# Performance work log

Hardware: AMD Instinct MI355X
Metric: run time of the kernel (lower is better)

## Reference

```python
import jax, jax.numpy as jnp
import numpy as np

B, QL, VL, HID, NH, CH = 16, 512, 512, 1024, 4, 10
DIM = HID // NH  # 256


def setup_inputs() -> dict:
    key = jax.random.key(0)
    ks = jax.random.split(key, 16)
    n = lambda k, s, sc=0.02: jax.random.normal(k, s, jnp.float32) * sc
    return {
        "query": jax.random.normal(ks[0], (B, QL, HID), jnp.float32),
        "value": jax.random.normal(ks[1], (B, VL, HID), jnp.float32),
        "prev_attn": jax.nn.softmax(jax.random.normal(ks[2], (B * NH, VL), jnp.float32), axis=-1),
        "conv_w": n(ks[3], (CH, 1, 3)),          # conv1d weight (out, in, k)
        "conv_b": jnp.zeros((CH,), jnp.float32),
        "Wq": n(ks[4], (HID, HID)), "bq": jnp.zeros((HID,), jnp.float32),  # query_projection
        "Wv": n(ks[5], (HID, HID)),               # value_projection (no bias)
        "Wloc": n(ks[6], (CH, DIM)),              # loc_projection (no bias)
        "bias": jax.random.uniform(ks[7], (HID,), jnp.float32, -0.1, 0.1),
        "Wout": n(ks[8], (2 * HID, HID)), "bout": jnp.zeros((HID,), jnp.float32),
        "swq": n(ks[9], (DIM, DIM)), "sbq": jnp.zeros((DIM,), jnp.float32),
        "swk": n(ks[10], (DIM, DIM)), "sbk": jnp.zeros((DIM,), jnp.float32),
        "swv": n(ks[11], (DIM, DIM)), "sbv": jnp.zeros((DIM,), jnp.float32),
    }


def _forward(query, value, prev_attn, conv_w, conv_b, Wq, bq, Wv, Wloc, bias,
             Wout, bout, swq, sbq, swk, sbk, swv, sbv):
    # location energy: conv1d over prev alignment, then per-head linear
    conv = jax.lax.conv_general_dilated(
        prev_attn[:, None, :], conv_w, window_strides=(1,), padding=((1, 1),),
        dimension_numbers=("NCH", "OIH", "NCH")) + conv_b[None, :, None]  # (B*NH, CH, VL)
    conv = conv.reshape(B, NH, CH, VL).transpose(0, 1, 3, 2)              # (B, NH, VL, CH)
    loc = jnp.einsum("bhvc,cd->bhvd", conv, Wloc)                         # (B, NH, VL, DIM)
    loc = loc.transpose(0, 2, 1, 3).reshape(B, VL, HID)                   # (B, VL, HID)

    q = query @ Wq + bq                                                   # (B, QL, HID)
    v = value @ Wv + loc + bias                                           # (B, VL, HID)

    # split heads: (B, L, NH, DIM) -> (NH*B, L, DIM)
    qh = q.reshape(B, QL, NH, DIM).transpose(2, 0, 1, 3).reshape(NH * B, QL, DIM)
    vh = v.reshape(B, VL, NH, DIM).transpose(2, 0, 1, 3).reshape(NH * B, VL, DIM)

    # scaled dot-product attention with key = value = vh (intended call)
    qq = qh @ swq + sbq
    kk = vh @ swk + sbk
    vv = vh @ swv + sbv
    scores = jnp.einsum("nqd,nkd->nqk", qq, kk) / np.float32(np.sqrt(DIM))
    attn = jax.nn.softmax(scores, axis=-1)                                # (NH*B, QL, VL)
    ctx = jnp.einsum("nqk,nkd->nqd", attn, vv)

    # merge heads: (NH, B, QL, DIM) -> (B, QL, HID)
    ctx = ctx.reshape(NH, B, QL, DIM).transpose(1, 2, 0, 3).reshape(B, QL, HID)

    combined = jnp.concatenate([ctx, query], axis=2)                      # (B, QL, 2*HID)
    out = jnp.tanh(combined @ Wout + bout)                                # (B, QL, HID)
    return out, attn


def reference(query, value, prev_attn, conv_w, conv_b, Wq, bq, Wv, Wloc, bias,
              Wout, bout, swq, sbq, swk, sbk, swv, sbv):
    return _forward(query, value, prev_attn, conv_w, conv_b, Wq, bq, Wv, Wloc,
                    bias, Wout, bout, swq, sbq, swk, sbk, swv, sbv)
```

## Files before the change

kernel.cpp:

```cpp
#include <hip/hip_runtime.h>
#include <math.h>

#define B_   16
#define QL_  512
#define VL_  512
#define HID_ 1024
#define NH_  4
#define CH_  10
#define DIM_ 256

typedef __attribute__((ext_vector_type(4))) float f32x4;
typedef __attribute__((ext_vector_type(8))) short bf16x8;

__device__ __forceinline__ ushort f2bf(float f) {
    union { float f; uint32_t u; } c; c.f = f;
    uint32_t u = c.u;
    u += 0x7fffu + ((u >> 16) & 1u);
    return (ushort)(u >> 16);
}

__device__ __forceinline__ void gload16(const void* g, void* l) {
    __builtin_amdgcn_global_load_lds((const __attribute__((address_space(1))) void*)g,
                                     (__attribute__((address_space(3))) void*)l,
                                     16, 0, 0);
}

__global__ __launch_bounds__(256)
void gemm_bf16(const ushort* __restrict__ A, const ushort* __restrict__ Bt,
               void* __restrict__ Cv, void* __restrict__ Cv2,
               const float* __restrict__ bias,
               int K, int lda, int ldb, int ldc,
               long long a1, long long a2, long long b1, long long b2,
               long long c1, long long c2, int WB,
               float post_scale, int flags)
{
    __shared__ ushort As[2][128 * 64];
    __shared__ ushort Bs[2][128 * 64];

    int z = blockIdx.z;
    int zm = z % WB, zd = z / WB;
    A  += a1 * zm + a2 * zd;
    Bt += b1 * zm + b2 * zd;
    long long coff = c1 * (long long)zm + c2 * (long long)zd;

    int gx = gridDim.x;
    int nwg = gx * gridDim.y;
    int flat = blockIdx.y * gx + blockIdx.x;
    int q = nwg >> 3, r = nwg & 7;
    int xcd = flat & 7, idx = flat >> 3;
    int logical = (xcd < r ? xcd * (q + 1) : r * (q + 1) + (xcd - r) * q) + idx;
    int brow = (logical / gx) * 128;
    int bcol = (logical % gx) * 128;

    int t = threadIdx.x;
    int lane = t & 63, w = t >> 6;
    int wr = (w >> 1) * 64, wc = (w & 1) * 64;

    int srow  = t >> 3;
    int sslot = t & 7;
    int sk = ((sslot ^ (srow & 7)) << 3);
    const ushort* gaBase = A  + (long long)(brow + srow) * lda + sk;
    const ushort* gbBase = Bt + (long long)(bcol + srow) * ldb + sk;

    f32x4 acc[4][4] = {};

    auto stage = [&](int buf, int k0) {
        ushort* la = &As[buf][t * 8];
        ushort* lb = &Bs[buf][t * 8];
        #pragma unroll
        for (int i = 0; i < 4; ++i) {
            gload16(gaBase + (long long)(i * 32) * lda + k0, la + i * 2048);
            gload16(gbBase + (long long)(i * 32) * ldb + k0, lb + i * 2048);
        }
    };

    int NT = K >> 6;
    stage(0, 0);
    __syncthreads();
    int cur = 0;
    for (int tI = 0; tI < NT; ++tI) {
        if (tI + 1 < NT) stage(cur ^ 1, (tI + 1) << 6);
        #pragma unroll
        for (int kk = 0; kk < 2; ++kk) {
            int slot = ((kk << 2) + (lane >> 4)) ^ (lane & 7);
            const ushort* ab = &As[cur][(wr + (lane & 15)) * 64 + slot * 8];
            const ushort* bb = &Bs[cur][(wc + (lane & 15)) * 64 + slot * 8];
            bf16x8 af[4], bfr[4];
            #pragma unroll
            for (int m = 0; m < 4; ++m) af[m]  = *(const bf16x8*)(ab + m * 1024);
            #pragma unroll
            for (int n = 0; n < 4; ++n) bfr[n] = *(const bf16x8*)(bb + n * 1024);
            #pragma unroll
            for (int m = 0; m < 4; ++m)
                #pragma unroll
                for (int n = 0; n < 4; ++n)
                    acc[m][n] = __builtin_amdgcn_mfma_f32_16x16x32_bf16(af[m], bfr[n], acc[m][n], 0, 0, 0);
        }
        __syncthreads();
        cur ^= 1;
    }

    float*  Cf = (float*)Cv + coff;
    ushort* Cb = (ushort*)Cv + coff;
    ushort* C2 = (ushort*)Cv2;
    #pragma unroll
    for (int m = 0; m < 4; ++m) {
        int r0 = brow + wr + m * 16 + (lane >> 4) * 4;
        #pragma unroll
        for (int n = 0; n < 4; ++n) {
            int c = bcol + wc + n * 16 + (lane & 15);
            float bv = bias ? bias[c] : 0.0f;
            float v0 = (acc[m][n][0] + bv) * post_scale;
            float v1 = (acc[m][n][1] + bv) * post_scale;
            float v2 = (acc[m][n][2] + bv) * post_scale;
            float v3 = (acc[m][n][3] + bv) * post_scale;
            if (flags & 2) { v0 = tanhf(v0); v1 = tanhf(v1); v2 = tanhf(v2); v3 = tanhf(v3); }
            if ((flags & 8) && c >= 1024) {
                ushort4 o;
                o.x = f2bf(v0); o.y = f2bf(v1); o.z = f2bf(v2); o.w = f2bf(v3);
                *(ushort4*)&C2[(long long)(c - 1024) * 8192 + r0] = o;
            } else if (flags & 1) {
                Cb[(long long)(r0 + 0) * ldc + c] = f2bf(v0);
                Cb[(long long)(r0 + 1) * ldc + c] = f2bf(v1);
                Cb[(long long)(r0 + 2) * ldc + c] = f2bf(v2);
                Cb[(long long)(r0 + 3) * ldc + c] = f2bf(v3);
            } else {
                Cf[(long long)(r0 + 0) * ldc + c] = v0;
                Cf[(long long)(r0 + 1) * ldc + c] = v1;
                Cf[(long long)(r0 + 2) * ldc + c] = v2;
                Cf[(long long)(r0 + 3) * ldc + c] = v3;
            }
        }
    }
}

__global__ __launch_bounds__(256)
void vext_fill_conv(const float* __restrict__ prev, const float* __restrict__ cw,
                    const float* __restrict__ cb, ushort* __restrict__ vext)
{
    int idx = blockIdx.x * 256 + threadIdx.x;
    int row = idx >> 6, j = idx & 63;
    int b = row >> 9, l = row & 511;
    ushort v = 0;
    if (j < 40) {
        int h = j / 10, c = j - h * 10;
        const float* p = prev + (long long)(b * 4 + h) * VL_;
        float xm = (l > 0)       ? p[l - 1] : 0.f;
        float x0 = p[l];
        float xp = (l < VL_ - 1) ? p[l + 1] : 0.f;
        v = f2bf(xm * cw[c * 3 + 0] + x0 * cw[c * 3 + 1] + xp * cw[c * 3 + 2] + cb[c]);
    }
    vext[(long long)row * 1088 + 1024 + j] = v;
}

__global__ __launch_bounds__(256)
void fold_small(const float* __restrict__ bq, const float* __restrict__ sbq, const float* __restrict__ swq,
                const float* __restrict__ bias, const float* __restrict__ sbk, const float* __restrict__ swk,
                const float* __restrict__ sbv, const float* __restrict__ swv,
                const float* __restrict__ Wloc,
                float* __restrict__ bqq, float* __restrict__ bkv,
                float* __restrict__ wlK, float* __restrict__ wlV)
{
    int idx = blockIdx.x * 256 + threadIdx.x;
    if (idx < 1024) {
        int h = idx >> 8, d = idx & 255;
        float s = 0.f;
        for (int j = 0; j < 256; ++j) s += bq[h * 256 + j] * swq[j * 256 + d];
        bqq[idx] = s + sbq[d];
    } else if (idx < 3072) {
        int i = idx - 1024;
        int kv = i >> 10, ii = i & 1023;
        int h = ii >> 8, d = ii & 255;
        const float* sw = kv ? swv : swk;
        const float* sb = kv ? sbv : sbk;
        float s = 0.f;
        for (int j = 0; j < 256; ++j) s += bias[h * 256 + j] * sw[j * 256 + d];
        bkv[i] = s + sb[d];
    } else if (idx < 5632) {
        int i = idx - 3072; int c = i >> 8, d = i & 255;
        float s = 0.f;
        for (int j = 0; j < 256; ++j) s += Wloc[c * 256 + j] * swk[j * 256 + d];
        wlK[i] = s;
    } else if (idx < 8192) {
        int i = idx - 5632; int c = i >> 8, d = i & 255;
        float s = 0.f;
        for (int j = 0; j < 256; ++j) s += Wloc[c * 256 + j] * swv[j * 256 + d];
        wlV[i] = s;
    }
}

__global__ __launch_bounds__(256)
void cast_rows(const float* __restrict__ in, ushort* __restrict__ out, int ld_out)
{
    long long idx = (long long)blockIdx.x * 256 + threadIdx.x;
    long long row = idx >> 8;
    int c4 = (int)(idx & 255) * 4;
    float4 v = *(const float4*)&in[row * 1024 + c4];
    ushort4 o;
    o.x = f2bf(v.x); o.y = f2bf(v.y); o.z = f2bf(v.z); o.w = f2bf(v.w);
    *(ushort4*)&out[row * ld_out + c4] = o;
}

__global__ __launch_bounds__(256)
void transpose_cast(const float* __restrict__ in, ushort* __restrict__ out, int R, int C, int ld_out)
{
    __shared__ float tile[64][65];
    int r0 = blockIdx.y * 64, c0 = blockIdx.x * 64;
    int t = threadIdx.x;
    int tr = t >> 2, tc = (t & 3) * 16;
    const float* ip = in + (long long)(r0 + tr) * C + c0 + tc;
    #pragma unroll
    for (int i = 0; i < 4; ++i) {
        float4 v = *(const float4*)(ip + i * 4);
        tile[tr][tc + i * 4 + 0] = v.x;
        tile[tr][tc + i * 4 + 1] = v.y;
        tile[tr][tc + i * 4 + 2] = v.z;
        tile[tr][tc + i * 4 + 3] = v.w;
    }
    __syncthreads();
    int cl = t >> 2, rl = (t & 3) * 16;
    ushort* op = out + (long long)(c0 + cl) * ld_out + r0 + rl;
    #pragma unroll
    for (int i = 0; i < 16; ++i) op[i] = f2bf(tile[rl + i][cl]);
}

__global__ __launch_bounds__(256)
void sw3_transpose(const float* __restrict__ swq, const float* __restrict__ swk,
                   const float* __restrict__ swv, ushort* __restrict__ oq,
                   ushort* __restrict__ ok, ushort* __restrict__ ov)
{
    __shared__ float tile[64][65];
    const float* in = (blockIdx.z == 0) ? swq : (blockIdx.z == 1) ? swk : swv;
    ushort* out     = (blockIdx.z == 0) ? oq  : (blockIdx.z == 1) ? ok  : ov;
    int r0 = blockIdx.y * 64, c0 = blockIdx.x * 64;
    int t = threadIdx.x;
    int tr = t >> 2, tc = (t & 3) * 16;
    const float* ip = in + (long long)(r0 + tr) * 256 + c0 + tc;
    #pragma unroll
    for (int i = 0; i < 4; ++i) {
        float4 v = *(const float4*)(ip + i * 4);
        tile[tr][tc + i * 4 + 0] = v.x;
        tile[tr][tc + i * 4 + 1] = v.y;
        tile[tr][tc + i * 4 + 2] = v.z;
        tile[tr][tc + i * 4 + 3] = v.w;
    }
    __syncthreads();
    int cl = t >> 2, rl = (t & 3) * 16;
    ushort* op = out + (long long)(c0 + cl) * 256 + r0 + rl;
    #pragma unroll
    for (int i = 0; i < 16; ++i) op[i] = f2bf(tile[rl + i][cl]);
}

__global__ __launch_bounds__(256)
void btext_fill(const float* __restrict__ wlK, const float* __restrict__ wlV,
                ushort* __restrict__ btExt)
{
    int idx = blockIdx.x * 256 + threadIdx.x;
    int n = idx >> 6, j = idx & 63;
    ushort v = 0;
    if (j < 40) {
        int hp = j / 10, c = j - hp * 10;
        int nn = n & 1023;
        int h = nn >> 8, d = nn & 255;
        if (hp == h) {
            const float* wl = (n >= 1024) ? wlV : wlK;
            v = f2bf(wl[c * 256 + d]);
        }
    }
    btExt[(long long)n * 1088 + 1024 + j] = v;
}

__global__ __launch_bounds__(256)
void softmax_rows(float* __restrict__ s, ushort* __restrict__ sb)
{
    long long row = blockIdx.x;
    float* p = s + row * (long long)VL_;
    int t = threadIdx.x;
    float2 v = *(float2*)(p + 2 * t);

    float m = fmaxf(v.x, v.y);
    #pragma unroll
    for (int o = 32; o > 0; o >>= 1) m = fmaxf(m, __shfl_down(m, o));
    __shared__ float redm[4];
    __shared__ float reds[4];
    int wave = t >> 6, lane = t & 63;
    if (lane == 0) redm[wave] = m;
    __syncthreads();
    if (t == 0) redm[0] = fmaxf(fmaxf(redm[0], redm[1]), fmaxf(redm[2], redm[3]));
    __syncthreads();
    m = redm[0];

    float e0 = __expf(v.x - m), e1 = __expf(v.y - m);
    float sum = e0 + e1;
    #pragma unroll
    for (int o = 32; o > 0; o >>= 1) sum += __shfl_down(sum, o);
    if (lane == 0) reds[wave] = sum;
    __syncthreads();
    if (t == 0) reds[0] = reds[0] + reds[1] + reds[2] + reds[3];
    __syncthreads();
    float inv = 1.0f / reds[0];

    float2 o2;
    o2.x = e0 * inv;
    o2.y = e1 * inv;
    *(float2*)(p + 2 * t) = o2;
    ushort2 ob;
    ob.x = f2bf(o2.x); ob.y = f2bf(o2.y);
    *(ushort2*)&sb[row * VL_ + 2 * t] = ob;
}

extern "C" void kernel_launch(void* const* d_in, const int* in_sizes, int n_in,
                              void* d_out, int out_size, void* d_ws, size_t ws_size,
                              hipStream_t stream)
{
    (void)in_sizes; (void)n_in; (void)out_size; (void)ws_size;

    const float* query = (const float*)d_in[0];
    const float* value = (const float*)d_in[1];
    const float* prev  = (const float*)d_in[2];
    const float* convw = (const float*)d_in[3];
    const float* convb = (const float*)d_in[4];
    const float* Wq    = (const float*)d_in[5];
    const float* bq    = (const float*)d_in[6];
    const float* Wv    = (const float*)d_in[7];
    const float* Wloc  = (const float*)d_in[8];
    const float* bias  = (const float*)d_in[9];
    const float* Wout  = (const float*)d_in[10];
    const float* bout  = (const float*)d_in[11];
    const float* swq   = (const float*)d_in[12];
    const float* sbq   = (const float*)d_in[13];
    const float* swk   = (const float*)d_in[14];
    const float* sbk   = (const float*)d_in[15];
    const float* swv   = (const float*)d_in[16];
    const float* sbv   = (const float*)d_in[17];

    float* out_buf  = (float*)d_out;
    float* attn_buf = out_buf + (long long)B_ * QL_ * HID_;

    char* wsb = (char*)d_ws;
    ushort* vext   = (ushort*)(wsb + 0);
    ushort* WoutTb = (ushort*)(wsb + 0);
    ushort* kkb    = (ushort*)(wsb + 17825792);
    ushort* attnb  = (ushort*)(wsb + 17825792);
    ushort* Acat   = (ushort*)(wsb + 51380224);
    ushort* qqb    = (ushort*)(wsb + 84934656);
    ushort* vvT_b  = (ushort*)(wsb + 101711872);
    float*  bqq    = (float*)(wsb + 118983424);
    float*  bkv    = (float*)(wsb + 118987520);
    float*  wlK    = (float*)(wsb + 118995712);
    float*  wlV    = (float*)(wsb + 119005952);
    ushort* swqTb  = (ushort*)(wsb + 119016192);
    ushort* swkTb  = (ushort*)(wsb + 119147264);
    ushort* swvTb  = (ushort*)(wsb + 119278336);
    ushort* Wqb    = (ushort*)(wsb + 119409408);
    ushort* Wvb    = (ushort*)(wsb + 121506560);
    ushort* wqqTb  = (ushort*)(wsb + 123603712);
    ushort* btExt  = (ushort*)(wsb + 125700864);

    fold_small<<<32, 256, 0, stream>>>(bq, sbq, swq, bias, sbk, swk, sbv, swv, Wloc,
                                       bqq, bkv, wlK, wlV);
    vext_fill_conv<<<2048, 256, 0, stream>>>(prev, convw, convb, vext);
    cast_rows<<<1024, 256, 0, stream>>>(Wq, Wqb, 1024);
    cast_rows<<<1024, 256, 0, stream>>>(Wv, Wvb, 1024);
    sw3_transpose<<<dim3(4, 4, 3), 256, 0, stream>>>(swq, swk, swv, swqTb, swkTb, swvTb);
    cast_rows<<<8192, 256, 0, stream>>>(query, Acat + 1024, 2048);
    cast_rows<<<8192, 256, 0, stream>>>(value, vext, 1088);

    gemm_bf16<<<dim3(8, 2, 4), 256, 0, stream>>>(swqTb, Wqb, wqqTb, nullptr, nullptr,
        256, 256, 1024, 1024, 0, 0, 0, 256, 0, 262144, 1, 1.0f, 1);
    gemm_bf16<<<dim3(8, 2, 4), 256, 0, stream>>>(swkTb, Wvb, btExt, nullptr, nullptr,
        256, 256, 1024, 1088, 0, 0, 0, 256, 0, 278528, 1, 1.0f, 1);
    gemm_bf16<<<dim3(8, 2, 4), 256, 0, stream>>>(swvTb, Wvb, btExt + (long long)1024 * 1088, nullptr, nullptr,
        256, 256, 1024, 1088, 0, 0, 0, 256, 0, 278528, 1, 1.0f, 1);
    btext_fill<<<512, 256, 0, stream>>>(wlK, wlV, btExt);

    gemm_bf16<<<dim3(8, 64, 1), 256, 0, stream>>>(Acat + 1024, wqqTb, qqb, nullptr, bqq,
        1024, 2048, 1024, 1024, 0, 0, 0, 0, 0, 0, 1, 0.0625f, 1);

    gemm_bf16<<<dim3(16, 64, 1), 256, 0, stream>>>(vext, btExt, kkb, vvT_b, bkv,
        1088, 1088, 1088, 1024, 0, 0, 0, 0, 0, 0, 1, 1.0f, 1 | 8);

    transpose_cast<<<dim3(16, 32), 256, 0, stream>>>(Wout, WoutTb, 2048, 1024, 2048);

    gemm_bf16<<<dim3(4, 4, 64), 256, 0, stream>>>(qqb, kkb, attn_buf, nullptr, nullptr,
        256, 1024, 1024, 512,
        524288, 256, 524288, 256, 262144, 4194304, 16, 1.0f, 0);

    softmax_rows<<<32768, 256, 0, stream>>>(attn_buf, attnb);

    gemm_bf16<<<dim3(2, 4, 64), 256, 0, stream>>>(attnb, vvT_b, Acat, nullptr, nullptr,
        512, 512, 8192, 2048,
        262144, 4194304, 512, 2097152, 1048576, 256, 16, 1.0f, 1);

    gemm_bf16<<<dim3(8, 64, 1), 256, 0, stream>>>(Acat, WoutTb, out_buf, nullptr, bout,
        2048, 2048, 2048, 1024, 0, 0, 0, 0, 0, 0, 1, 1.0f, 2);
}
```

Before: 300.7 us.

## Add 256x256-tile GEMM kernel with XCD-aware block remap for large projections

Adds a new bf16 MFMA GEMM kernel with 256x256 output tiles, 512 threads, K-step 32, double-buffered LDS fills through global_load_lds with an XOR swizzle, and a workgroup remap that keeps neighbouring tiles on the same XCD. The query projection, the fused key/value projection and the output projection now use it in place of the 128x128 kernel. The aim is more data reuse per tile and better L2 locality. The cost is fewer workgroups (128 or 256), which may leave CUs underused, and the larger accumulator arrays raise register pressure.

```diff
diff --git a/kernel.cpp b/kernel.cpp
--- a/kernel.cpp
+++ b/kernel.cpp
@@ -23,6 +23,112 @@
     __builtin_amdgcn_global_load_lds((const __attribute__((address_space(1))) void*)g,
                                      (__attribute__((address_space(3))) void*)l,
                                      16, 0, 0);
+}
+
+__global__ __launch_bounds__(512, 2)
+void gemm256(const ushort* __restrict__ A, const ushort* __restrict__ Bt,
+             void* __restrict__ Cv, void* __restrict__ Cv2,
+             const float* __restrict__ bias,
+             int K, int lda, int ldb, int ldc,
+             float post_scale, int flags)
+{
+    __shared__ ushort As[2][256 * 32];
+    __shared__ ushort Bs[2][256 * 32];
+
+    int gx = gridDim.x, nwg = gx * gridDim.y;
+    int flat = blockIdx.y * gx + blockIdx.x;
+    int q = nwg >> 3, r = nwg & 7;
+    int xcd = flat & 7, idx = flat >> 3;
+    int logical = (xcd < r ? xcd * (q + 1) : r * (q + 1) + (xcd - r) * q) + idx;
+    int brow = (logical / gx) * 256;
+    int bcol = (logical % gx) * 256;
+
+    int t = threadIdx.x;
+    int lane = t & 63, w = t >> 6;
+    int wr = (w >> 2) * 128;
+    int wc = (w & 3) * 64;
+
+    int srow  = t >> 2;
+    int sslot = t & 3;
+    int sk = ((sslot ^ ((srow >> 1) & 3)) << 3);
+    const ushort* ga0 = A  + (long long)(brow + srow) * lda + sk;
+    const ushort* ga1 = A  + (long long)(brow + 128 + srow) * lda + sk;
+    const ushort* gb0 = Bt + (long long)(bcol + srow) * ldb + sk;
+    const ushort* gb1 = Bt + (long long)(bcol + 128 + srow) * ldb + sk;
+
+    f32x4 acc[8][4] = {};
+
+    auto stage = [&](int buf, int k0) {
+        gload16(ga0 + k0, &As[buf][t * 8]);
+        gload16(ga1 + k0, &As[buf][4096 + t * 8]);
+        gload16(gb0 + k0, &Bs[buf][t * 8]);
+        gload16(gb1 + k0, &Bs[buf][4096 + t * 8]);
+    };
+
+    int NT = K >> 5;
+    stage(0, 0);
+    int cur = 0;
+    for (int tI = 0; tI < NT; ++tI) {
+        if (tI + 1 < NT) {
+            stage(cur ^ 1, (tI + 1) << 5);
+            asm volatile("s_waitcnt vmcnt(4)" ::: "memory");
+        } else {
+            asm volatile("s_waitcnt vmcnt(0)" ::: "memory");
+        }
+        __builtin_amdgcn_s_barrier();
+        __builtin_amdgcn_sched_barrier(0);
+
+        int slot = (lane >> 4) ^ ((lane >> 1) & 3);
+        const ushort* ab = &As[cur][(wr + (lane & 15)) * 32 + slot * 8];
+        const ushort* bb = &Bs[cur][(wc + (lane & 15)) * 32 + slot * 8];
+        bf16x8 af[8], bfr[4];
+        #pragma unroll
+        for (int m = 0; m < 8; ++m) af[m]  = *(const bf16x8*)(ab + m * 512);
+        #pragma unroll
+        for (int n = 0; n < 4; ++n) bfr[n] = *(const bf16x8*)(bb + n * 512);
+        #pragma unroll
+        for (int m = 0; m < 8; ++m)
+            #pragma unroll
+            for (int n = 0; n < 4; ++n)
+                acc[m][n] = __builtin_amdgcn_mfma_f32_16x16x32_bf16(af[m], bfr[n], acc[m][n], 0, 0, 0);
+
+        __builtin_amdgcn_s_barrier();
+        __builtin_amdgcn_sched_barrier(0);
+        cur ^= 1;
+    }
+
+    float*  Cf = (float*)Cv;
+    ushort* Cb = (ushort*)Cv;
+    ushort* C2 = (ushort*)Cv2;
+    #pragma unroll
+    for (int m = 0; m < 8; ++m) {
+        int r0 = brow + wr + m * 16 + (lane >> 4) * 4;
+        #pragma unroll
+        for (int n = 0; n < 4; ++n) {
+            int c = bcol + wc + n * 16 + (lane & 15);
+            float bv = bias ? bias[c] : 0.0f;
+            float v0 = (acc[m][n][0] + bv) * post_scale;
+            float v1 = (acc[m][n][1] + bv) * post_scale;
+            float v2 = (acc[m][n][2] + bv) * post_scale;
+            float v3 = (acc[m][n][3] + bv) * post_scale;
+            if (flags & 2) { v0 = tanhf(v0); v1 = tanhf(v1); v2 = tanhf(v2); v3 = tanhf(v3); }
+            if ((flags & 8) && c >= 1024) {
+                ushort4 o;
+                o.x = f2bf(v0); o.y = f2bf(v1); o.z = f2bf(v2); o.w = f2bf(v3);
+                *(ushort4*)&C2[(long long)(c - 1024) * 8192 + r0] = o;
+            } else if (flags & 1) {
+                Cb[(long long)(r0 + 0) * ldc + c] = f2bf(v0);
+                Cb[(long long)(r0 + 1) * ldc + c] = f2bf(v1);
+                Cb[(long long)(r0 + 2) * ldc + c] = f2bf(v2);
+                Cb[(long long)(r0 + 3) * ldc + c] = f2bf(v3);
+            } else {
+                Cf[(long long)(r0 + 0) * ldc + c] = v0;
+                Cf[(long long)(r0 + 1) * ldc + c] = v1;
+                Cf[(long long)(r0 + 2) * ldc + c] = v2;
+                Cf[(long long)(r0 + 3) * ldc + c] = v3;
+            }
+        }
+    }
 }
 
 __global__ __launch_bounds__(256)
@@ -374,11 +480,11 @@
         256, 256, 1024, 1088, 0, 0, 0, 256, 0, 278528, 1, 1.0f, 1);
     btext_fill<<<512, 256, 0, stream>>>(wlK, wlV, btExt);
 
-    gemm_bf16<<<dim3(8, 64, 1), 256, 0, stream>>>(Acat + 1024, wqqTb, qqb, nullptr, bqq,
-        1024, 2048, 1024, 1024, 0, 0, 0, 0, 0, 0, 1, 0.0625f, 1);
-
-    gemm_bf16<<<dim3(16, 64, 1), 256, 0, stream>>>(vext, btExt, kkb, vvT_b, bkv,
-        1088, 1088, 1088, 1024, 0, 0, 0, 0, 0, 0, 1, 1.0f, 1 | 8);
+    gemm256<<<dim3(4, 32), 512, 0, stream>>>(Acat + 1024, wqqTb, qqb, nullptr, bqq,
+        1024, 2048, 1024, 1024, 0.0625f, 1);
+
+    gemm256<<<dim3(8, 32), 512, 0, stream>>>(vext, btExt, kkb, vvT_b, bkv,
+        1088, 1088, 1088, 1024, 1.0f, 1 | 8);
 
     transpose_cast<<<dim3(16, 32), 256, 0, stream>>>(Wout, WoutTb, 2048, 1024, 2048);
 
@@ -392,6 +498,6 @@
         512, 512, 8192, 2048,
         262144, 4194304, 512, 2097152, 1048576, 256, 16, 1.0f, 1);
 
-    gemm_bf16<<<dim3(8, 64, 1), 256, 0, stream>>>(Acat, WoutTb, out_buf, nullptr, bout,
-        2048, 2048, 2048, 1024, 0, 0, 0, 0, 0, 0, 1, 1.0f, 2);
-}
+    gemm256<<<dim3(4, 32), 512, 0, stream>>>(Acat, WoutTb, out_buf, nullptr, bout,
+        2048, 2048, 2048, 1024, 1.0f, 2);
+}
```

After: 398.6 us. 1.33x slower.

## Fuse score GEMM with row softmax in a single full-row kernel

Applied to the files above, without the earlier changes.

Replaces the separate QK^T GEMM and the softmax_rows kernel with one kernel in which each 512-thread block computes a 128x512 score tile and does the row max, exp and normalization in registers via shuffles and shared memory. This avoids writing fp32 scores to global memory and reading them back for softmax. Workspace offsets are shifted so attnb no longer aliases kkb, since kk is still being read while attnb is written. The grid is only 256 blocks with one block per CU and a large accumulator footprint, so occupancy and latency hiding may suffer.

```diff
diff --git a/kernel.cpp b/kernel.cpp
--- a/kernel.cpp
+++ b/kernel.cpp
@@ -129,6 +129,125 @@
                 Cf[(long long)(r0 + 1) * ldc + c] = v1;
                 Cf[(long long)(r0 + 2) * ldc + c] = v2;
                 Cf[(long long)(r0 + 3) * ldc + c] = v3;
+            }
+        }
+    }
+}
+
+__global__ __launch_bounds__(512, 1)
+void scores_softmax(const ushort* __restrict__ qq, const ushort* __restrict__ kk,
+                    float* __restrict__ attn, ushort* __restrict__ attnb)
+{
+    __shared__ ushort As[128 * 32];
+    __shared__ ushort Bs[512 * 32];
+    __shared__ float redm[4][128];
+    __shared__ float reds[4][128];
+
+    int z = blockIdx.z;
+    int b = z & 15, h = z >> 4;
+    const ushort* Abase = qq + (long long)b * 524288 + h * 256;
+    const ushort* Bbase = kk + (long long)b * 524288 + h * 256;
+    float*  aout = attn  + (long long)z * 262144;
+    ushort* bout = attnb + (long long)z * 262144;
+
+    int brow = blockIdx.y * 128;
+
+    int t = threadIdx.x;
+    int lane = t & 63, w = t >> 6;
+    int wr = (w >> 2) * 64;
+    int wc = (w & 3) * 128;
+
+    int srow = t >> 2, sslot = t & 3;
+    int sk = ((sslot ^ ((srow >> 1) & 3)) << 3);
+    const ushort* ga = Abase + (long long)(brow + srow) * 1024 + sk;
+    const ushort* gb = Bbase + (long long)srow * 1024 + sk;
+
+    f32x4 acc[4][8] = {};
+
+    for (int k0 = 0; k0 < 256; k0 += 32) {
+        gload16(ga + k0, &As[t * 8]);
+        #pragma unroll
+        for (int i = 0; i < 4; ++i)
+            gload16(gb + (long long)(i * 128) * 1024 + k0, &Bs[t * 8 + i * 4096]);
+        __syncthreads();
+
+        int slot = (lane >> 4) ^ ((lane >> 1) & 3);
+        const ushort* ab = &As[(wr + (lane & 15)) * 32 + slot * 8];
+        const ushort* bb = &Bs[(wc + (lane & 15)) * 32 + slot * 8];
+        bf16x8 af[4], bfr[8];
+        #pragma unroll
+        for (int m = 0; m < 4; ++m) af[m]  = *(const bf16x8*)(ab + m * 512);
+        #pragma unroll
+        for (int n = 0; n < 8; ++n) bfr[n] = *(const bf16x8*)(bb + n * 512);
+        #pragma unroll
+        for (int m = 0; m < 4; ++m)
+            #pragma unroll
+            for (int n = 0; n < 8; ++n)
+                acc[m][n] = __builtin_amdgcn_mfma_f32_16x16x32_bf16(af[m], bfr[n], acc[m][n], 0, 0, 0);
+        __syncthreads();
+    }
+
+    float rmax[4][4], rinv[4][4];
+    #pragma unroll
+    for (int m = 0; m < 4; ++m)
+        #pragma unroll
+        for (int j = 0; j < 4; ++j) {
+            float pm = acc[m][0][j];
+            #pragma unroll
+            for (int n = 1; n < 8; ++n) pm = fmaxf(pm, acc[m][n][j]);
+            pm = fmaxf(pm, __shfl_xor(pm, 1));
+            pm = fmaxf(pm, __shfl_xor(pm, 2));
+            pm = fmaxf(pm, __shfl_xor(pm, 4));
+            pm = fmaxf(pm, __shfl_xor(pm, 8));
+            if ((lane & 15) == 0)
+                redm[w & 3][wr + m * 16 + (lane >> 4) * 4 + j] = pm;
+        }
+    __syncthreads();
+    #pragma unroll
+    for (int m = 0; m < 4; ++m)
+        #pragma unroll
+        for (int j = 0; j < 4; ++j) {
+            int row = wr + m * 16 + (lane >> 4) * 4 + j;
+            rmax[m][j] = fmaxf(fmaxf(redm[0][row], redm[1][row]),
+                               fmaxf(redm[2][row], redm[3][row]));
+        }
+    #pragma unroll
+    for (int m = 0; m < 4; ++m)
+        #pragma unroll
+        for (int j = 0; j < 4; ++j) {
+            float ps = 0.f;
+            #pragma unroll
+            for (int n = 0; n < 8; ++n) {
+                float e = __expf(acc[m][n][j] - rmax[m][j]);
+                acc[m][n][j] = e;
+                ps += e;
+            }
+            ps += __shfl_xor(ps, 1);
+            ps += __shfl_xor(ps, 2);
+            ps += __shfl_xor(ps, 4);
+            ps += __shfl_xor(ps, 8);
+            if ((lane & 15) == 0)
+                reds[w & 3][wr + m * 16 + (lane >> 4) * 4 + j] = ps;
+        }
+    __syncthreads();
+    #pragma unroll
+    for (int m = 0; m < 4; ++m)
+        #pragma unroll
+        for (int j = 0; j < 4; ++j) {
+            int row = wr + m * 16 + (lane >> 4) * 4 + j;
+            rinv[m][j] = 1.0f / (reds[0][row] + reds[1][row] + reds[2][row] + reds[3][row]);
+        }
+    #pragma unroll
+    for (int m = 0; m < 4; ++m) {
+        int r0 = brow + wr + m * 16 + (lane >> 4) * 4;
+        #pragma unroll
+        for (int n = 0; n < 8; ++n) {
+            int c = wc + n * 16 + (lane & 15);
+            #pragma unroll
+            for (int j = 0; j < 4; ++j) {
+                float v = acc[m][n][j] * rinv[m][j];
+                aout[(long long)(r0 + j) * 512 + c] = v;
+                bout[(long long)(r0 + j) * 512 + c] = f2bf(v);
             }
         }
     }
@@ -270,45 +389,6 @@
     btExt[(long long)n * 1088 + 1024 + j] = v;
 }
 
-__global__ __launch_bounds__(256)
-void softmax_rows(float* __restrict__ s, ushort* __restrict__ sb)
-{
-    long long row = blockIdx.x;
-    float* p = s + row * (long long)VL_;
-    int t = threadIdx.x;
-    float2 v = *(float2*)(p + 2 * t);
-
-    float m = fmaxf(v.x, v.y);
-    #pragma unroll
-    for (int o = 32; o > 0; o >>= 1) m = fmaxf(m, __shfl_down(m, o));
-    __shared__ float redm[4];
-    __shared__ float reds[4];
-    int wave = t >> 6, lane = t & 63;
-    if (lane == 0) redm[wave] = m;
-    __syncthreads();
-    if (t == 0) redm[0] = fmaxf(fmaxf(redm[0], redm[1]), fmaxf(redm[2], redm[3]));
-    __syncthreads();
-    m = redm[0];
-
-    float e0 = __expf(v.x - m), e1 = __expf(v.y - m);
-    float sum = e0 + e1;
-    #pragma unroll
-    for (int o = 32; o > 0; o >>= 1) sum += __shfl_down(sum, o);
-    if (lane == 0) reds[wave] = sum;
-    __syncthreads();
-    if (t == 0) reds[0] = reds[0] + reds[1] + reds[2] + reds[3];
-    __syncthreads();
-    float inv = 1.0f / reds[0];
-
-    float2 o2;
-    o2.x = e0 * inv;
-    o2.y = e1 * inv;
-    *(float2*)(p + 2 * t) = o2;
-    ushort2 ob;
-    ob.x = f2bf(o2.x); ob.y = f2bf(o2.y);
-    *(ushort2*)&sb[row * VL_ + 2 * t] = ob;
-}
-
 extern "C" void kernel_launch(void* const* d_in, const int* in_sizes, int n_in,
                               void* d_out, int out_size, void* d_ws, size_t ws_size,
                               hipStream_t stream)
@@ -341,21 +421,21 @@
     ushort* vext   = (ushort*)(wsb + 0);
     ushort* WoutTb = (ushort*)(wsb + 0);
     ushort* kkb    = (ushort*)(wsb + 17825792);
-    ushort* attnb  = (ushort*)(wsb + 17825792);
-    ushort* Acat   = (ushort*)(wsb + 51380224);
-    ushort* qqb    = (ushort*)(wsb + 84934656);
-    ushort* vvT_b  = (ushort*)(wsb + 101711872);
-    float*  bqq    = (float*)(wsb + 118983424);
-    float*  bkv    = (float*)(wsb + 118987520);
-    float*  wlK    = (float*)(wsb + 118995712);
-    float*  wlV    = (float*)(wsb + 119005952);
-    ushort* swqTb  = (ushort*)(wsb + 119016192);
-    ushort* swkTb  = (ushort*)(wsb + 119147264);
-    ushort* swvTb  = (ushort*)(wsb + 119278336);
-    ushort* Wqb    = (ushort*)(wsb + 119409408);
-    ushort* Wvb    = (ushort*)(wsb + 121506560);
-    ushort* wqqTb  = (ushort*)(wsb + 123603712);
-    ushort* btExt  = (ushort*)(wsb + 125700864);
+    ushort* attnb  = (ushort*)(wsb + 34603008);
+    ushort* Acat   = (ushort*)(wsb + 68157440);
+    ushort* qqb    = (ushort*)(wsb + 101711872);
+    ushort* vvT_b  = (ushort*)(wsb + 118489088);
+    float*  bqq    = (float*)(wsb + 135266304);
+    float*  bkv    = (float*)(wsb + 135270400);
+    float*  wlK    = (float*)(wsb + 135278592);
+    float*  wlV    = (float*)(wsb + 135288832);
+    ushort* swqTb  = (ushort*)(wsb + 135299072);
+    ushort* swkTb  = (ushort*)(wsb + 135430144);
+    ushort* swvTb  = (ushort*)(wsb + 135561216);
+    ushort* Wqb    = (ushort*)(wsb + 135692288);
+    ushort* Wvb    = (ushort*)(wsb + 137789440);
+    ushort* wqqTb  = (ushort*)(wsb + 139886592);
+    ushort* btExt  = (ushort*)(wsb + 141983744);
 
     fold_small<<<32, 256, 0, stream>>>(bq, sbq, swq, bias, sbk, swk, sbv, swv, Wloc,
                                        bqq, bkv, wlK, wlV);
@@ -382,11 +462,7 @@
 
     transpose_cast<<<dim3(16, 32), 256, 0, stream>>>(Wout, WoutTb, 2048, 1024, 2048);
 
-    gemm_bf16<<<dim3(4, 4, 64), 256, 0, stream>>>(qqb, kkb, attn_buf, nullptr, nullptr,
-        256, 1024, 1024, 512,
-        524288, 256, 524288, 256, 262144, 4194304, 16, 1.0f, 0);
-
-    softmax_rows<<<32768, 256, 0, stream>>>(attn_buf, attnb);
+    scores_softmax<<<dim3(1, 4, 64), 512, 0, stream>>>(qqb, kkb, attn_buf, attnb);
 
     gemm_bf16<<<dim3(2, 4, 64), 256, 0, stream>>>(attnb, vvT_b, Acat, nullptr, nullptr,
         512, 512, 8192, 2048,
```

Result: faster. 286.5 us (-4.7%).
